# Kernel tuning notes

Hardware: AMD Instinct MI355X
Metric: run time of the kernel (lower is better)

Reference implementation:

```python
import jax, jax.numpy as jnp
import numpy as np
from jax import lax

B, T, H, W, C = 2, 32, 65, 65, 32
KS = 15   # kernel_size
F = 32    # conv features


def setup_inputs() -> dict:
    key = jax.random.key(0)
    ks = jax.random.split(key, 12)
    d = {}
    d["input_seq"] = jax.random.normal(ks[0], (B, T, H, W, C), jnp.float32)
    d["conv_w"] = jax.random.normal(ks[1], (3, 3, C, F), jnp.float32) / np.sqrt(3 * 3 * C).astype(np.float32)
    d["conv_b"] = jnp.zeros((F,), jnp.float32)
    for i, nm in enumerate(["alpha", "delta", "mu", "gamma"]):
        d[f"w_{nm}"] = jax.random.normal(ks[2 + i], (F, C), jnp.float32) / np.sqrt(F).astype(np.float32)
        d[f"b_{nm}"] = jnp.zeros((C,), jnp.float32)
    # nn.initializers.normal() -> stddev 0.01
    d["k_exc"] = jax.random.normal(ks[10], (KS, KS, C), jnp.float32) * 0.01
    d["k_inh"] = jax.random.normal(ks[11], (KS, KS, C), jnp.float32) * 0.01
    return d


def _kernel_spec(k, Hh, Ww):
    # zero-pad the (KS,KS,C) kernel to (H,W,C), then rfft2 over spatial axes
    ph, pw = (Hh - KS) // 2, (Ww - KS) // 2
    kp = jnp.pad(k, ((ph, ph), (pw, pw), (0, 0)))
    return jnp.fft.rfft2(kp, axes=(0, 1))  # (H, W//2+1, C) complex64


def reference(input_seq, conv_w, conv_b, w_alpha, b_alpha, w_delta, b_delta,
              w_mu, b_mu, w_gamma, b_gamma, k_exc, k_inh):
    Bb, Tt, Hh, Ww, Cc = input_seq.shape
    # context conv: flax Conv flattens leading (B,T) into batch; SAME, stride 2
    x = input_seq.reshape(Bb * Tt, Hh, Ww, Cc)
    stats = lax.conv_general_dilated(x, conv_w, (2, 2), 'SAME',
                                     dimension_numbers=('NHWC', 'HWIO', 'NHWC')) + conv_b
    stats = jax.nn.gelu(stats)  # flax nn.gelu (approximate)
    Hp, Wp = stats.shape[1], stats.shape[2]
    stats = stats.reshape(Bb, Tt, Hp, Wp, F)
    ctx = jnp.mean(stats, axis=(1, 2))                 # (B, Wp, F); Wp == W//2+1 for odd W
    alpha = jax.nn.sigmoid(ctx @ w_alpha + b_alpha)    # (B, Wp, C)
    delta = jax.nn.sigmoid(ctx @ w_delta + b_delta)
    mu = jax.nn.softplus(ctx @ w_mu + b_mu)
    gamma = jax.nn.softplus(ctx @ w_gamma + b_gamma)

    K_E = _kernel_spec(k_exc, Hh, Ww)  # (H, Wr, C)
    K_I = _kernel_spec(k_inh, Hh, Ww)
    Wr = Ww // 2 + 1
    decay = jnp.asarray(0.9, jnp.complex64)

    bc = lambda v: jnp.broadcast_to(v[:, None, :, :].astype(jnp.complex64), (Bb, Hh, Wr, Cc))
    A_xx = decay * bc(alpha)
    A_yy = decay * bc(delta)
    A_xy = -K_I[None] * bc(mu)
    A_yx = K_E[None] * bc(gamma)
    row0 = jnp.stack([A_xx, A_xy], axis=-1)
    row1 = jnp.stack([A_yx, A_yy], axis=-1)
    K_hat = jnp.stack([row0, row1], axis=-2)           # (B, H, Wr, C, 2, 2)

    U_hat = jnp.fft.rfft2(input_seq, axes=(2, 3))      # (B, T, H, Wr, C) complex64
    U_vec = jnp.stack([U_hat, jnp.zeros_like(U_hat)], axis=-1)  # (B,T,H,Wr,C,2)
    A_t = jnp.broadcast_to(K_hat[:, None], (Bb, Tt, Hh, Wr, Cc, 2, 2))

    # associative op for linear SSM: state_t = A_t @ state_{t-1} + u_t
    # (log/exp of the original cancel: exp(log A)=A, exp(State_log)=State)
    def combine(l, r):
        A1, b1 = l
        A2, b2 = r
        A = jnp.einsum('...ij,...jk->...ik', A2, A1)
        b = jnp.einsum('...ij,...j->...i', A2, b1) + b2
        return A, b

    _, S = lax.associative_scan(combine, (A_t, U_vec), axis=1)
    Y = S[..., 1]                                      # inhibitory component
    return jnp.fft.irfft2(Y, axes=(2, 3))              # (B, T, H, 2*(Wr-1), C) float32
```

## Files before the change

kernel.cpp:

```cpp
#include <hip/hip_runtime.h>
#include <cmath>

#define NB 2
#define NT 32
#define NH 65
#define NW 65
#define NC 32
#define NF 32
#define NKS 15
#define NHP 33
#define NWP 33
#define NWR 33
#define NWOUT 64
#define PI_F 3.14159265358979323846f

using bf16x8 = __attribute__((ext_vector_type(8))) __bf16;
using f32x4  = __attribute__((ext_vector_type(4))) float;
using s16x4  = __attribute__((ext_vector_type(4))) short;

__device__ inline unsigned short f2bf(float v) {
    unsigned u = __float_as_uint(v);
    u = u + 0x7FFF + ((u >> 16) & 1);
    return (unsigned short)(u >> 16);
}
__device__ inline float bf2f(unsigned short h) {
    return __uint_as_float((unsigned)h << 16);
}

union FragU { s16x4 h[2]; bf16x8 v; };

__global__ __launch_bounds__(256) void setup_kernel(
    const float* __restrict__ w, unsigned short* __restrict__ wBh,
    unsigned short* __restrict__ wBl,
    float2* __restrict__ twr, float2* __restrict__ twb, float2* __restrict__ twi,
    const float* __restrict__ kexc, const float* __restrict__ kinh,
    float2* __restrict__ KE, float2* __restrict__ KI)
{
    int blk = blockIdx.x;
    if (blk < 10) {
        int tid = blk * 256 + threadIdx.x;
        if (tid < NH * 36) {
            int q = tid / 36, wr = tid % 36;
            float2 v = make_float2(0.f, 0.f);
            if (wr < NWR) {
                int p = (q * wr) % NH;
                float a = -2.f * PI_F * (float)p / (float)NH;
                v = make_float2(cosf(a), sinf(a));
            }
            twr[tid] = v;
        }
        if (tid < NH * 14) {
            int h = tid / 14, b = tid % 14;
            float2 v = make_float2(0.f, 0.f);
            if (b < 13) {
                int p = (h * b) % NH;
                float a = 2.f * PI_F * (float)p / (float)NH;
                v = make_float2(cosf(a), sinf(a));
            }
            twb[tid] = v;
        }
        if (tid < 31 * 64) {
            int q = tid / 64 + 1, ow = tid % 64;
            int p = (q * ow) & 63;
            float a = 2.f * PI_F * (float)p / (float)NWOUT;
            twi[tid] = make_float2(cosf(a), sinf(a));
        }
    } else if (blk < 46) {
        int tid = (blk - 10) * 256 + threadIdx.x;
        if (tid < 9 * NF * NC) {
            int dd = tid / 1024;
            int f = (tid / 32) % 32;
            int c = tid % 32;
            float v = w[((size_t)dd * NC + c) * NF + f];
            unsigned short h = f2bf(v);
            wBh[tid] = h;
            wBl[tid] = f2bf(v - bf2f(h));
        }
    } else {
        __shared__ float2 tw[NH];
        int tid = threadIdx.x;
        if (tid < NH) {
            float a = -2.f * PI_F * (float)tid / (float)NH;
            tw[tid] = make_float2(cosf(a), sinf(a));
        }
        __syncthreads();
        int idx = (blk - 46) * 256 + tid;
        if (idx >= NH * NWR * NC) return;
        int c = idx % NC;
        int rem = idx / NC;
        int wr = rem % NWR;
        int h = rem / NWR;
        float ker = 0, kei = 0, kir = 0, kii = 0;
        int prow = (25 * (h + wr)) % NH;
        for (int i = 0; i < NKS; ++i) {
            int p = prow;
            for (int j = 0; j < NKS; ++j) {
                float2 e = tw[p];
                float ve = kexc[(i * NKS + j) * NC + c];
                float vi = kinh[(i * NKS + j) * NC + c];
                ker = fmaf(ve, e.x, ker); kei = fmaf(ve, e.y, kei);
                kir = fmaf(vi, e.x, kir); kii = fmaf(vi, e.y, kii);
                p += wr; if (p >= NH) p -= NH;
            }
            prow += h; if (prow >= NH) prow -= NH;
        }
        KE[idx] = make_float2(ker, kei);
        KI[idx] = make_float2(kir, kii);
    }
}

__global__ __launch_bounds__(256) void conv_mfma_kernel(
    const float* __restrict__ x, const unsigned short* __restrict__ wBh,
    const unsigned short* __restrict__ wBl, const float* __restrict__ bias,
    float* __restrict__ partial)
{
    __shared__ unsigned short aH[3 * 68 * 36];
    __shared__ unsigned short aL[3 * 68 * 36];
    int blk = blockIdx.x;
    int i = blk % NHP;
    int bt = blk / NHP;
    int tid = threadIdx.x;
    int l = tid & 63;
    int w = tid >> 6;

    int nt = w & 1;
    int fcol = nt * 16 + (l & 15);
    int c0 = (l >> 4) * 8;
    bf16x8 bh[9], bl[9];
    #pragma unroll
    for (int dd = 0; dd < 9; ++dd) {
        bh[dd] = *(const bf16x8*)(wBh + dd * 1024 + fcol * 32 + c0);
        bl[dd] = *(const bf16x8*)(wBl + dd * 1024 + fcol * 32 + c0);
    }

    const float* xb = x + (size_t)bt * (NH * NW * NC);
    for (int q = tid; q < 3 * 68 * 8; q += 256) {
        int r = q / 544;
        int k = q % 544;
        int pcol = k >> 3;
        int c4 = (k & 7) * 4;
        int gr = 2 * i - 1 + r;
        int gcol = pcol - 1;
        float4 v = make_float4(0.f, 0.f, 0.f, 0.f);
        if (gr >= 0 && gr < NH && gcol >= 0 && gcol < NW)
            v = *(const float4*)(xb + ((size_t)gr * NW + gcol) * NC + c4);
        int base = (r * 68 + pcol) * 36 + c4;
        unsigned short h0 = f2bf(v.x), h1 = f2bf(v.y), h2 = f2bf(v.z), h3 = f2bf(v.w);
        s16x4 th = {(short)h0, (short)h1, (short)h2, (short)h3};
        *(s16x4*)(aH + base) = th;
        s16x4 tl = {(short)f2bf(v.x - bf2f(h0)), (short)f2bf(v.y - bf2f(h1)),
                    (short)f2bf(v.z - bf2f(h2)), (short)f2bf(v.w - bf2f(h3))};
        *(s16x4*)(aL + base) = tl;
    }
    __syncthreads();

    float bv = bias[fcol];
    f32x4 acc0 = {bv, bv, bv, bv};
    f32x4 acc1 = {bv, bv, bv, bv};
    const int mtA = (w >> 1) ? 1 : 0;
    const bool hasB = (w >> 1) == 0;
    int m15 = l & 15;

    #pragma unroll
    for (int dd = 0; dd < 9; ++dd) {
        const int di = dd / 3, dj = dd % 3;
        {
            int pcol = 2 * (mtA * 16 + m15) + dj;
            int off = (di * 68 + pcol) * 36 + c0;
            FragU ah, al;
            ah.h[0] = *(const s16x4*)(aH + off);
            ah.h[1] = *(const s16x4*)(aH + off + 4);
            al.h[0] = *(const s16x4*)(aL + off);
            al.h[1] = *(const s16x4*)(aL + off + 4);
            acc0 = __builtin_amdgcn_mfma_f32_16x16x32_bf16(al.v, bh[dd], acc0, 0, 0, 0);
            acc0 = __builtin_amdgcn_mfma_f32_16x16x32_bf16(ah.v, bl[dd], acc0, 0, 0, 0);
            acc0 = __builtin_amdgcn_mfma_f32_16x16x32_bf16(ah.v, bh[dd], acc0, 0, 0, 0);
        }
        if (hasB) {
            int pcol = 2 * (32 + m15) + dj;
            if (pcol > 67) pcol = 67;
            int off = (di * 68 + pcol) * 36 + c0;
            FragU ah, al;
            ah.h[0] = *(const s16x4*)(aH + off);
            ah.h[1] = *(const s16x4*)(aH + off + 4);
            al.h[0] = *(const s16x4*)(aL + off);
            al.h[1] = *(const s16x4*)(aL + off + 4);
            acc1 = __builtin_amdgcn_mfma_f32_16x16x32_bf16(al.v, bh[dd], acc1, 0, 0, 0);
            acc1 = __builtin_amdgcn_mfma_f32_16x16x32_bf16(ah.v, bl[dd], acc1, 0, 0, 0);
            acc1 = __builtin_amdgcn_mfma_f32_16x16x32_bf16(ah.v, bh[dd], acc1, 0, 0, 0);
        }
    }

    float* pout = partial + (size_t)blk * (NWP * NF);
    int g4 = (l >> 4) * 4;
    #define GELU(v) (0.5f * (v) * (1.f + tanhf(0.7978845608028654f * ((v) + 0.044715f * (v) * (v) * (v)))))
    #pragma unroll
    for (int r = 0; r < 4; ++r) {
        float v = acc0[r];
        pout[(mtA * 16 + g4 + r) * NF + fcol] = GELU(v);
    }
    if (hasB && g4 == 0) {
        float v = acc1[0];
        pout[32 * NF + fcol] = GELU(v);
    }
    #undef GELU
}

__global__ __launch_bounds__(256) void ctx_reduce1_kernel(
    const float* __restrict__ partial, float* __restrict__ red2)
{
    __shared__ float red[4][64];
    int blk = blockIdx.x;
    int b = blk / 136;
    int rem = blk % 136;
    int chunk = rem / 8;
    int ts = rem % 8;
    int lane = threadIdx.x & 63;
    int tig = threadIdx.x >> 6;
    int jf = chunk * 64 + lane;
    float s0 = 0.f, s1 = 0.f, s2 = 0.f;
    if (jf < NWP * NF) {
        const float* p = partial + (size_t)b * (NT * NHP) * (NWP * NF)
                       + (size_t)(ts * 132 + tig * 33) * (NWP * NF) + jf;
        #pragma unroll 3
        for (int s = 0; s < 33; s += 3) {
            s0 += p[(size_t)s * (NWP * NF)];
            s1 += p[(size_t)(s + 1) * (NWP * NF)];
            s2 += p[(size_t)(s + 2) * (NWP * NF)];
        }
    }
    red[tig][lane] = s0 + s1 + s2;
    __syncthreads();
    if (threadIdx.x < 64) {
        float tot = red[0][threadIdx.x] + red[1][threadIdx.x] +
                    red[2][threadIdx.x] + red[3][threadIdx.x];
        red2[((b * 17 + chunk) * 8 + ts) * 64 + threadIdx.x] = tot;
    }
}

__global__ __launch_bounds__(256) void ctx_reduce2_kernel(
    const float* __restrict__ red2, float* __restrict__ ctx)
{
    __shared__ float red[4][64];
    int b = blockIdx.x / 17, chunk = blockIdx.x % 17;
    int lane = threadIdx.x & 63, tg = threadIdx.x >> 6;
    const float* r2 = red2 + ((size_t)(b * 17 + chunk) * 8) * 64;
    float v = r2[(2 * tg) * 64 + lane] + r2[(2 * tg + 1) * 64 + lane];
    red[tg][lane] = v;
    __syncthreads();
    if (threadIdx.x < 64) {
        int jf = chunk * 64 + threadIdx.x;
        if (jf < NWP * NF) {
            float tot = red[0][threadIdx.x] + red[1][threadIdx.x] +
                        red[2][threadIdx.x] + red[3][threadIdx.x];
            ctx[b * (NWP * NF) + jf] = tot * (1.f / (NT * NHP));
        }
    }
}

__global__ __launch_bounds__(256) void gate_kernel(
    const float* __restrict__ ctx,
    const float* __restrict__ wA, const float* __restrict__ bA,
    const float* __restrict__ wD, const float* __restrict__ bD,
    const float* __restrict__ wM, const float* __restrict__ bM,
    const float* __restrict__ wG, const float* __restrict__ bG,
    float* __restrict__ alpha, float* __restrict__ delta,
    float* __restrict__ mu, float* __restrict__ gamma)
{
    int idx = blockIdx.x * 256 + threadIdx.x;
    if (idx >= NB * NWP * NC) return;
    int c = idx % NC;
    int bw = idx / NC;
    float sA = bA[c], sD = bD[c], sM = bM[c], sG = bG[c];
    #pragma unroll
    for (int f = 0; f < NF; ++f) {
        float v = ctx[bw * NF + f];
        sA = fmaf(v, wA[f * NC + c], sA);
        sD = fmaf(v, wD[f * NC + c], sD);
        sM = fmaf(v, wM[f * NC + c], sM);
        sG = fmaf(v, wG[f * NC + c], sG);
    }
    alpha[idx] = 1.f / (1.f + expf(-sA));
    delta[idx] = 1.f / (1.f + expf(-sD));
    mu[idx]    = fmaxf(sM, 0.f) + log1pf(expf(-fabsf(sM)));
    gamma[idx] = fmaxf(sG, 0.f) + log1pf(expf(-fabsf(sG)));
}

__global__ __launch_bounds__(256) void dft_rows_kernel(
    const float* __restrict__ x, const float2* __restrict__ twr_g,
    float2* __restrict__ U1)
{
    __shared__ __align__(16) float row[4][NW * NC];
    __shared__ __align__(16) float2 twt[NH * 36];
    int tid = threadIdx.x;
    int blk = blockIdx.x;
    int grp = blk % 17;
    int bt = blk / 17;
    int hbase = grp * 4;
    int nrows = NH - hbase; if (nrows > 4) nrows = 4;

    const float* xp = x + ((size_t)bt * NH + hbase) * (NW * NC);
    for (int idx = tid; idx < nrows * NW * NC; idx += 256) ((float*)row)[idx] = xp[idx];
    for (int idx = tid; idx < NH * 36; idx += 256) twt[idx] = twr_g[idx];
    __syncthreads();

    int c = tid & 31;
    int jg = tid >> 5;
    float2 acc[4][4];
    #pragma unroll
    for (int r = 0; r < 4; ++r)
        #pragma unroll
        for (int k = 0; k < 4; ++k) acc[r][k] = make_float2(0.f, 0.f);

    const float2* tp = twt + 4 * jg;
    #pragma unroll 5
    for (int q = 0; q < NW; ++q) {
        float4 e01 = *(const float4*)&tp[q * 36];
        float4 e23 = *(const float4*)&tp[q * 36 + 2];
        #pragma unroll
        for (int r = 0; r < 4; ++r) {
            float v = row[r][q * NC + c];
            acc[r][0].x = fmaf(v, e01.x, acc[r][0].x); acc[r][0].y = fmaf(v, e01.y, acc[r][0].y);
            acc[r][1].x = fmaf(v, e01.z, acc[r][1].x); acc[r][1].y = fmaf(v, e01.w, acc[r][1].y);
            acc[r][2].x = fmaf(v, e23.x, acc[r][2].x); acc[r][2].y = fmaf(v, e23.y, acc[r][2].y);
            acc[r][3].x = fmaf(v, e23.z, acc[r][3].x); acc[r][3].y = fmaf(v, e23.w, acc[r][3].y);
        }
    }
    #pragma unroll
    for (int r = 0; r < 4; ++r) {
        if (r < nrows) {
            float2* up = U1 + ((size_t)bt * NH + hbase + r) * (NWR * NC);
            up[(4 * jg + 0) * NC + c] = acc[r][0];
            up[(4 * jg + 1) * NC + c] = acc[r][1];
            up[(4 * jg + 2) * NC + c] = acc[r][2];
            up[(4 * jg + 3) * NC + c] = acc[r][3];
        }
    }
    if (jg == 0) {
        float2 a32[4];
        #pragma unroll
        for (int r = 0; r < 4; ++r) a32[r] = make_float2(0.f, 0.f);
        #pragma unroll 5
        for (int q = 0; q < NW; ++q) {
            float2 e = twt[q * 36 + 32];
            #pragma unroll
            for (int r = 0; r < 4; ++r) {
                float v = row[r][q * NC + c];
                a32[r].x = fmaf(v, e.x, a32[r].x);
                a32[r].y = fmaf(v, e.y, a32[r].y);
            }
        }
        #pragma unroll
        for (int r = 0; r < 4; ++r)
            if (r < nrows)
                U1[((size_t)bt * NH + hbase + r) * (NWR * NC) + 32 * NC + c] = a32[r];
    }
}

template <int SIGN>
__device__ inline void compute5(const float2 v[5], float2* outp) {
    const float C5[5] = {1.f, 0.30901699437494742f, -0.80901699437494745f,
                         -0.80901699437494745f, 0.30901699437494742f};
    const float S5[5] = {0.f, 0.95105651629515357f, 0.58778525229247314f,
                         -0.58778525229247314f, -0.95105651629515357f};
    #pragma unroll
    for (int r = 0; r < 5; ++r) {
        float re = 0.f, im = 0.f;
        #pragma unroll
        for (int a = 0; a < 5; ++a) {
            const int m = (r * a) % 5;
            const float ex = C5[m];
            const float ey = (float)SIGN * S5[m];
            re = fmaf(v[a].x, ex, fmaf(-v[a].y, ey, re));
            im = fmaf(v[a].x, ey, fmaf(v[a].y, ex, im));
        }
        outp[r * NC] = make_float2(re, im);
    }
}

template <int SIGN, bool SCALE>
__global__ __launch_bounds__(256) void dft_cols_kernel(
    const float2* __restrict__ in, float2* __restrict__ out,
    const float2* __restrict__ twb_g)
{
    __shared__ __align__(16) float2 col[NH * NC];
    __shared__ __align__(16) float2 twb[NH * 14];
    int tid = threadIdx.x;
    int blk = blockIdx.x;
    int wr = blk % NWR;
    int bt = blk / NWR;
    const float2* ip = in + ((size_t)bt * NH) * (NWR * NC) + wr * NC;
    for (int idx = tid; idx < NH * NC; idx += 256) {
        int p = idx >> 5, c = idx & 31;
        col[idx] = ip[(size_t)p * (NWR * NC) + c];
    }
    for (int idx = tid; idx < NH * 14; idx += 256) twb[idx] = twb_g[idx];
    __syncthreads();

    float2 va0[5], va1[5];
    int bq0 = tid >> 5, c0 = tid & 31;
    int q1 = tid + 256;
    int bq1 = q1 >> 5, c1 = q1 & 31;
    #pragma unroll
    for (int a = 0; a < 5; ++a) {
        va0[a] = col[(13 * a + bq0) * NC + c0];
        if (q1 < 416) va1[a] = col[(13 * a + bq1) * NC + c1];
    }
    __syncthreads();
    compute5<SIGN>(va0, &col[(bq0 * 5) * NC + c0]);
    if (q1 < 416) compute5<SIGN>(va1, &col[(bq1 * 5) * NC + c1]);
    __syncthreads();

    const float S = (float)SIGN;
    int c = tid & 31;
    int h0 = tid >> 5;
    const float s = SCALE ? (1.f / (float)NH) : 1.f;
    float2* op = out + ((size_t)bt * NH) * (NWR * NC) + wr * NC;
    float2 acc[8];
    #pragma unroll
    for (int k = 0; k < 8; ++k) {
        int h = h0 + 8 * k;
        int r = h % 5;
        const float2* Ap = col + r * NC + c;
        const float2* tp = twb + h * 14;
        float re = 0.f, im = 0.f;
        #pragma unroll
        for (int p = 0; p < 6; ++p) {
            float4 tq = *(const float4*)&tp[2 * p];
            float2 v0 = Ap[(2 * p) * 5 * NC];
            float2 v1 = Ap[(2 * p + 1) * 5 * NC];
            re = fmaf(v0.x, tq.x, fmaf(-S * v0.y, tq.y, re));
            im = fmaf(S * v0.x, tq.y, fmaf(v0.y, tq.x, im));
            re = fmaf(v1.x, tq.z, fmaf(-S * v1.y, tq.w, re));
            im = fmaf(S * v1.x, tq.w, fmaf(v1.y, tq.z, im));
        }
        {
            float2 t12 = tp[12];
            float2 v = Ap[12 * 5 * NC];
            re = fmaf(v.x, t12.x, fmaf(-S * v.y, t12.y, re));
            im = fmaf(S * v.x, t12.y, fmaf(v.y, t12.x, im));
        }
        acc[k] = make_float2(re * s, im * s);
    }
    #pragma unroll
    for (int k = 0; k < 8; ++k) {
        int h = h0 + 8 * k;
        op[(size_t)h * (NWR * NC) + c] = acc[k];
    }
    if (h0 == 0) {
        const float2* Ap = col + 4 * NC + c;
        const float2* tp = twb + 64 * 14;
        float re = 0.f, im = 0.f;
        #pragma unroll
        for (int p = 0; p < 6; ++p) {
            float4 tq = *(const float4*)&tp[2 * p];
            float2 v0 = Ap[(2 * p) * 5 * NC];
            float2 v1 = Ap[(2 * p + 1) * 5 * NC];
            re = fmaf(v0.x, tq.x, fmaf(-S * v0.y, tq.y, re));
            im = fmaf(S * v0.x, tq.y, fmaf(v0.y, tq.x, im));
            re = fmaf(v1.x, tq.z, fmaf(-S * v1.y, tq.w, re));
            im = fmaf(S * v1.x, tq.w, fmaf(v1.y, tq.z, im));
        }
        {
            float2 t12 = tp[12];
            float2 v = Ap[12 * 5 * NC];
            re = fmaf(v.x, t12.x, fmaf(-S * v.y, t12.y, re));
            im = fmaf(S * v.x, t12.y, fmaf(v.y, t12.x, im));
        }
        op[(size_t)64 * (NWR * NC) + c] = make_float2(re * s, im * s);
    }
}

__global__ __launch_bounds__(256) void scan_kernel(
    float2* __restrict__ buf, const float2* __restrict__ KE,
    const float2* __restrict__ KI, const float* __restrict__ alpha,
    const float* __restrict__ delta, const float* __restrict__ mu,
    const float* __restrict__ gamma)
{
    int idx = blockIdx.x * 256 + threadIdx.x;
    if (idx >= NB * NH * NWR * NC) return;
    int c = idx % NC;
    int rem = idx / NC;
    int wr = rem % NWR;
    int rem2 = rem / NWR;
    int h = rem2 % NH;
    int b = rem2 / NH;

    int gi = (b * NWP + wr) * NC + c;
    float axx = 0.9f * alpha[gi];
    float ayy = 0.9f * delta[gi];
    float m = mu[gi], g = gamma[gi];
    float2 ki = KI[(h * NWR + wr) * NC + c];
    float2 ke = KE[(h * NWR + wr) * NC + c];
    float2 axy = make_float2(-ki.x * m, -ki.y * m);
    float2 ayx = make_float2(ke.x * g, ke.y * g);

    float2 xs = make_float2(0.f, 0.f), ys = make_float2(0.f, 0.f);
    size_t base = ((size_t)b * NT) * NH * NWR * NC + (size_t)h * (NWR * NC) + wr * NC + c;
    const size_t stride = (size_t)NH * NWR * NC;
    for (int t = 0; t < NT; ++t) {
        float2 U = buf[base + (size_t)t * stride];
        float2 nx, ny;
        nx.x = fmaf(axx, xs.x, fmaf(axy.x, ys.x, fmaf(-axy.y, ys.y, U.x)));
        nx.y = fmaf(axx, xs.y, fmaf(axy.x, ys.y, fmaf(axy.y, ys.x, U.y)));
        ny.x = fmaf(ayx.x, xs.x, fmaf(-ayx.y, xs.y, ayy * ys.x));
        ny.y = fmaf(ayx.x, xs.y, fmaf(ayx.y, xs.x, ayy * ys.y));
        xs = nx; ys = ny;
        buf[base + (size_t)t * stride] = ys;
    }
}

__global__ __launch_bounds__(256) void irfft_w_kernel(
    const float2* __restrict__ Z, const float2* __restrict__ twi_g,
    float* __restrict__ out)
{
    __shared__ __align__(16) float2 z[4][NWR * NC];
    __shared__ __align__(16) float2 twi[31 * 64];
    int tid = threadIdx.x;
    int blk = blockIdx.x;
    int grp = blk % 17;
    int bt = blk / 17;
    int hbase = grp * 4;
    int nrows = NH - hbase; if (nrows > 4) nrows = 4;

    const float2* zp = Z + ((size_t)bt * NH + hbase) * (NWR * NC);
    for (int idx = tid; idx < nrows * NWR * NC; idx += 256) ((float2*)z)[idx] = zp[idx];
    for (int idx = tid; idx < 31 * 64; idx += 256) twi[idx] = twi_g[idx];
    __syncthreads();

    int c = tid & 31;
    int g = tid >> 5;
    float acc[4][8];
    #pragma unroll
    for (int r = 0; r < 4; ++r) {
        float z0 = z[r][c].x;
        float zn = z[r][32 * NC + c].x;
        #pragma unroll
        for (int m = 0; m < 8; ++m) acc[r][m] = z0 + ((m & 1) ? -zn : zn);
    }
    const float2* tp = twi + 8 * g;
    for (int q = 1; q < 32; ++q) {
        const float4* tq = (const float4*)&tp[(q - 1) * 64];
        float4 e0 = tq[0], e1 = tq[1], e2 = tq[2], e3 = tq[3];
        #pragma unroll
        for (int r = 0; r < 4; ++r) {
            float2 v = z[r][q * NC + c];
            float vx = 2.f * v.x, vy = 2.f * v.y;
            acc[r][0] = fmaf(vx, e0.x, fmaf(-vy, e0.y, acc[r][0]));
            acc[r][1] = fmaf(vx, e0.z, fmaf(-vy, e0.w, acc[r][1]));
            acc[r][2] = fmaf(vx, e1.x, fmaf(-vy, e1.y, acc[r][2]));
            acc[r][3] = fmaf(vx, e1.z, fmaf(-vy, e1.w, acc[r][3]));
            acc[r][4] = fmaf(vx, e2.x, fmaf(-vy, e2.y, acc[r][4]));
            acc[r][5] = fmaf(vx, e2.z, fmaf(-vy, e2.w, acc[r][5]));
            acc[r][6] = fmaf(vx, e3.x, fmaf(-vy, e3.y, acc[r][6]));
            acc[r][7] = fmaf(vx, e3.z, fmaf(-vy, e3.w, acc[r][7]));
        }
    }
    #pragma unroll
    for (int r = 0; r < 4; ++r) {
        if (r < nrows) {
            float* op = out + ((size_t)bt * NH + hbase + r) * (NWOUT * NC);
            #pragma unroll
            for (int m = 0; m < 8; ++m)
                op[(8 * g + m) * NC + c] = acc[r][m] * (1.f / (float)NWOUT);
        }
    }
}

extern "C" void kernel_launch(void* const* d_in, const int* in_sizes, int n_in,
                              void* d_out, int out_size, void* d_ws, size_t ws_size,
                              hipStream_t stream)
{
    const float* x     = (const float*)d_in[0];
    const float* convw = (const float*)d_in[1];
    const float* convb = (const float*)d_in[2];
    const float* wA = (const float*)d_in[3];
    const float* bA = (const float*)d_in[4];
    const float* wD = (const float*)d_in[5];
    const float* bD = (const float*)d_in[6];
    const float* wM = (const float*)d_in[7];
    const float* bM = (const float*)d_in[8];
    const float* wG = (const float*)d_in[9];
    const float* bG = (const float*)d_in[10];
    const float* kexc = (const float*)d_in[11];
    const float* kinh = (const float*)d_in[12];

    const size_t NBIG = (size_t)NB * NT * NH * NWR * NC;
    char* ws = (char*)d_ws;
    float2* bufA    = (float2*)ws;  ws += NBIG * sizeof(float2);
    float2* KE      = (float2*)ws;  ws += (size_t)NH * NWR * NC * sizeof(float2);
    float2* KI      = (float2*)ws;  ws += (size_t)NH * NWR * NC * sizeof(float2);
    float*  partial = (float*)ws;   ws += (size_t)NB * (NT * NHP) * (NWP * NF) * sizeof(float);
    float*  ctx     = (float*)ws;   ws += (size_t)NB * NWP * NF * sizeof(float);
    float*  red2    = (float*)ws;   ws += (size_t)NB * 17 * 8 * 64 * sizeof(float);
    float*  alpha   = (float*)ws;   ws += (size_t)NB * NWP * NC * sizeof(float);
    float*  delta   = (float*)ws;   ws += (size_t)NB * NWP * NC * sizeof(float);
    float*  mu      = (float*)ws;   ws += (size_t)NB * NWP * NC * sizeof(float);
    float*  gamma   = (float*)ws;   ws += (size_t)NB * NWP * NC * sizeof(float);
    float2* TWR     = (float2*)ws;  ws += (size_t)NH * 36 * sizeof(float2);
    float2* TWB     = (float2*)ws;  ws += (size_t)NH * 14 * sizeof(float2);
    float2* TWI     = (float2*)ws;  ws += (size_t)31 * 64 * sizeof(float2);
    unsigned short* wBh = (unsigned short*)ws; ws += (size_t)9 * NC * NF * sizeof(unsigned short);
    unsigned short* wBl = (unsigned short*)ws; ws += (size_t)9 * NC * NF * sizeof(unsigned short);

    const int specBlocks = (NH * NWR * NC + 255) / 256;
    setup_kernel<<<46 + specBlocks, 256, 0, stream>>>(
        convw, wBh, wBl, TWR, TWB, TWI, kexc, kinh, KE, KI);

    conv_mfma_kernel<<<NB * NT * NHP, 256, 0, stream>>>(x, wBh, wBl, convb, partial);
    ctx_reduce1_kernel<<<NB * 136, 256, 0, stream>>>(partial, red2);
    ctx_reduce2_kernel<<<NB * 17, 256, 0, stream>>>(red2, ctx);
    gate_kernel<<<(NB * NWP * NC + 255) / 256, 256, 0, stream>>>(
        ctx, wA, bA, wD, bD, wM, bM, wG, bG, alpha, delta, mu, gamma);

    dft_rows_kernel<<<NB * NT * 17, 256, 0, stream>>>(x, TWR, bufA);
    dft_cols_kernel<-1, false><<<NB * NT * NWR, 256, 0, stream>>>(bufA, bufA, TWB);

    scan_kernel<<<(NB * NH * NWR * NC + 255) / 256, 256, 0, stream>>>(
        bufA, KE, KI, alpha, delta, mu, gamma);

    dft_cols_kernel<+1, true><<<NB * NT * NWR, 256, 0, stream>>>(bufA, bufA, TWB);
    irfft_w_kernel<<<NB * NT * 17, 256, 0, stream>>>(bufA, TWI, (float*)d_out);
}
```

Before: 168.8 us.

## Replace column DFT with split-bf16 MFMA matrix multiply over 65-point axis

The hand-written 5x13 factored column DFT on CUDA cores is replaced by a dense DFT matmul on MFMA units. Setup precomputes hi/lo bf16 split tables of the cos and ±sin DFT matrix, padded to 80x96. Each block converts its column data into hi/lo bf16 in shared memory, and four waves compute 16x16 output tiles with three-product split-bf16 accumulation to keep near-fp32 accuracy. This trades more raw FLOPs (a dense DFT instead of a factored one, plus 12 MFMAs per k-tile) for tensor-core throughput. It also adds bf16 conversion overhead and some precision risk.

```diff
diff --git a/kernel.cpp b/kernel.cpp
--- a/kernel.cpp
+++ b/kernel.cpp
@@ -32,9 +32,10 @@
 __global__ __launch_bounds__(256) void setup_kernel(
     const float* __restrict__ w, unsigned short* __restrict__ wBh,
     unsigned short* __restrict__ wBl,
-    float2* __restrict__ twr, float2* __restrict__ twb, float2* __restrict__ twi,
+    float2* __restrict__ twr, float2* __restrict__ twi,
     const float* __restrict__ kexc, const float* __restrict__ kinh,
-    float2* __restrict__ KE, float2* __restrict__ KI)
+    float2* __restrict__ KE, float2* __restrict__ KI,
+    unsigned short* __restrict__ Atab)
 {
     int blk = blockIdx.x;
     if (blk < 10) {
@@ -49,16 +50,6 @@
             }
             twr[tid] = v;
         }
-        if (tid < NH * 14) {
-            int h = tid / 14, b = tid % 14;
-            float2 v = make_float2(0.f, 0.f);
-            if (b < 13) {
-                int p = (h * b) % NH;
-                float a = 2.f * PI_F * (float)p / (float)NH;
-                v = make_float2(cosf(a), sinf(a));
-            }
-            twb[tid] = v;
-        }
         if (tid < 31 * 64) {
             int q = tid / 64 + 1, ow = tid % 64;
             int p = (q * ow) & 63;
@@ -76,7 +67,7 @@
             wBh[tid] = h;
             wBl[tid] = f2bf(v - bf2f(h));
         }
-    } else {
+    } else if (blk < 315) {
         __shared__ float2 tw[NH];
         int tid = threadIdx.x;
         if (tid < NH) {
@@ -106,6 +97,27 @@
         }
         KE[idx] = make_float2(ker, kei);
         KI[idx] = make_float2(kir, kii);
+    } else {
+        int idx = (blk - 315) * 256 + threadIdx.x;
+        if (idx >= 46080) return;
+        int tbl = idx / 7680;
+        int rem = idx % 7680;
+        int mt = rem / 1536;
+        int rem2 = rem % 1536;
+        int kt = rem2 / 512;
+        int rem3 = rem2 % 512;
+        int lane = rem3 / 8;
+        int e = rem3 % 8;
+        int m = mt * 16 + (lane & 15);
+        int k = kt * 32 + (lane >> 4) * 8 + e;
+        unsigned short out = 0;
+        if (m < NH && k < NH) {
+            float a = 2.f * PI_F * (float)((m * k) % NH) / (float)NH;
+            float base = (tbl < 2) ? cosf(a) : ((tbl < 4) ? sinf(a) : -sinf(a));
+            unsigned short hi = f2bf(base);
+            out = (tbl & 1) ? f2bf(base - bf2f(hi)) : hi;
+        }
+        Atab[idx] = out;
     }
 }
 
@@ -357,117 +369,80 @@
     }
 }
 
-template <int SIGN>
-__device__ inline void compute5(const float2 v[5], float2* outp) {
-    const float C5[5] = {1.f, 0.30901699437494742f, -0.80901699437494745f,
-                         -0.80901699437494745f, 0.30901699437494742f};
-    const float S5[5] = {0.f, 0.95105651629515357f, 0.58778525229247314f,
-                         -0.58778525229247314f, -0.95105651629515357f};
-    #pragma unroll
-    for (int r = 0; r < 5; ++r) {
-        float re = 0.f, im = 0.f;
-        #pragma unroll
-        for (int a = 0; a < 5; ++a) {
-            const int m = (r * a) % 5;
-            const float ex = C5[m];
-            const float ey = (float)SIGN * S5[m];
-            re = fmaf(v[a].x, ex, fmaf(-v[a].y, ey, re));
-            im = fmaf(v[a].x, ey, fmaf(v[a].y, ex, im));
-        }
-        outp[r * NC] = make_float2(re, im);
-    }
-}
-
-template <int SIGN, bool SCALE>
-__global__ __launch_bounds__(256) void dft_cols_kernel(
+template <int DIR>
+__global__ __launch_bounds__(256) void dft_cols_mfma_kernel(
     const float2* __restrict__ in, float2* __restrict__ out,
-    const float2* __restrict__ twb_g)
-{
-    __shared__ __align__(16) float2 col[NH * NC];
-    __shared__ __align__(16) float2 twb[NH * 14];
+    const unsigned short* __restrict__ Atab)
+{
+    __shared__ __align__(16) unsigned short Xt[4][32][104];
     int tid = threadIdx.x;
     int blk = blockIdx.x;
     int wr = blk % NWR;
     int bt = blk / NWR;
     const float2* ip = in + ((size_t)bt * NH) * (NWR * NC) + wr * NC;
-    for (int idx = tid; idx < NH * NC; idx += 256) {
+
+    for (int idx = tid; idx < 96 * 32; idx += 256) {
         int p = idx >> 5, c = idx & 31;
-        col[idx] = ip[(size_t)p * (NWR * NC) + c];
-    }
-    for (int idx = tid; idx < NH * 14; idx += 256) twb[idx] = twb_g[idx];
+        float2 v = make_float2(0.f, 0.f);
+        if (p < NH) v = ip[(size_t)p * (NWR * NC) + c];
+        unsigned short rh = f2bf(v.x);
+        unsigned short ih = f2bf(v.y);
+        Xt[0][c][p] = rh;
+        Xt[1][c][p] = f2bf(v.x - bf2f(rh));
+        Xt[2][c][p] = ih;
+        Xt[3][c][p] = f2bf(v.y - bf2f(ih));
+    }
     __syncthreads();
 
-    float2 va0[5], va1[5];
-    int bq0 = tid >> 5, c0 = tid & 31;
-    int q1 = tid + 256;
-    int bq1 = q1 >> 5, c1 = q1 & 31;
-    #pragma unroll
-    for (int a = 0; a < 5; ++a) {
-        va0[a] = col[(13 * a + bq0) * NC + c0];
-        if (q1 < 416) va1[a] = col[(13 * a + bq1) * NC + c1];
-    }
-    __syncthreads();
-    compute5<SIGN>(va0, &col[(bq0 * 5) * NC + c0]);
-    if (q1 < 416) compute5<SIGN>(va1, &col[(bq1 * 5) * NC + c1]);
-    __syncthreads();
-
-    const float S = (float)SIGN;
-    int c = tid & 31;
-    int h0 = tid >> 5;
-    const float s = SCALE ? (1.f / (float)NH) : 1.f;
+    int l = tid & 63;
+    int w = tid >> 6;
+    int lm = l & 15;
+    int lk = (l >> 4) * 8;
+    const float scale = DIR ? (1.f / (float)NH) : 1.f;
     float2* op = out + ((size_t)bt * NH) * (NWR * NC) + wr * NC;
-    float2 acc[8];
-    #pragma unroll
-    for (int k = 0; k < 8; ++k) {
-        int h = h0 + 8 * k;
-        int r = h % 5;
-        const float2* Ap = col + r * NC + c;
-        const float2* tp = twb + h * 14;
-        float re = 0.f, im = 0.f;
-        #pragma unroll
-        for (int p = 0; p < 6; ++p) {
-            float4 tq = *(const float4*)&tp[2 * p];
-            float2 v0 = Ap[(2 * p) * 5 * NC];
-            float2 v1 = Ap[(2 * p + 1) * 5 * NC];
-            re = fmaf(v0.x, tq.x, fmaf(-S * v0.y, tq.y, re));
-            im = fmaf(S * v0.x, tq.y, fmaf(v0.y, tq.x, im));
-            re = fmaf(v1.x, tq.z, fmaf(-S * v1.y, tq.w, re));
-            im = fmaf(S * v1.x, tq.w, fmaf(v1.y, tq.z, im));
-        }
-        {
-            float2 t12 = tp[12];
-            float2 v = Ap[12 * 5 * NC];
-            re = fmaf(v.x, t12.x, fmaf(-S * v.y, t12.y, re));
-            im = fmaf(S * v.x, t12.y, fmaf(v.y, t12.x, im));
-        }
-        acc[k] = make_float2(re * s, im * s);
-    }
-    #pragma unroll
-    for (int k = 0; k < 8; ++k) {
-        int h = h0 + 8 * k;
-        op[(size_t)h * (NWR * NC) + c] = acc[k];
-    }
-    if (h0 == 0) {
-        const float2* Ap = col + 4 * NC + c;
-        const float2* tp = twb + 64 * 14;
-        float re = 0.f, im = 0.f;
-        #pragma unroll
-        for (int p = 0; p < 6; ++p) {
-            float4 tq = *(const float4*)&tp[2 * p];
-            float2 v0 = Ap[(2 * p) * 5 * NC];
-            float2 v1 = Ap[(2 * p + 1) * 5 * NC];
-            re = fmaf(v0.x, tq.x, fmaf(-S * v0.y, tq.y, re));
-            im = fmaf(S * v0.x, tq.y, fmaf(v0.y, tq.x, im));
-            re = fmaf(v1.x, tq.z, fmaf(-S * v1.y, tq.w, re));
-            im = fmaf(S * v1.x, tq.w, fmaf(v1.y, tq.z, im));
-        }
-        {
-            float2 t12 = tp[12];
-            float2 v = Ap[12 * 5 * NC];
-            re = fmaf(v.x, t12.x, fmaf(-S * v.y, t12.y, re));
-            im = fmaf(S * v.x, t12.y, fmaf(v.y, t12.x, im));
-        }
-        op[(size_t)64 * (NWR * NC) + c] = make_float2(re * s, im * s);
+
+    for (int pr = w; pr < 10; pr += 4) {
+        int mt = pr >> 1, nt = pr & 1;
+        f32x4 accr = {0.f, 0.f, 0.f, 0.f};
+        f32x4 acci = {0.f, 0.f, 0.f, 0.f};
+        #pragma unroll
+        for (int kt = 0; kt < 3; ++kt) {
+            const unsigned short* ab = Atab + ((size_t)mt * 3 + kt) * 512 + l * 8;
+            bf16x8 Ch  = *(const bf16x8*)(ab + 0 * 7680);
+            bf16x8 Cl  = *(const bf16x8*)(ab + 1 * 7680);
+            bf16x8 Sph = *(const bf16x8*)(ab + 2 * 7680);
+            bf16x8 Spl = *(const bf16x8*)(ab + 3 * 7680);
+            bf16x8 Snh = *(const bf16x8*)(ab + 4 * 7680);
+            bf16x8 Snl = *(const bf16x8*)(ab + 5 * 7680);
+            bf16x8 S1h = DIR ? Snh : Sph, S1l = DIR ? Snl : Spl;
+            bf16x8 S2h = DIR ? Sph : Snh, S2l = DIR ? Spl : Snl;
+            int n = nt * 16 + lm;
+            int k = kt * 32 + lk;
+            bf16x8 Xrh = *(const bf16x8*)&Xt[0][n][k];
+            bf16x8 Xrl = *(const bf16x8*)&Xt[1][n][k];
+            bf16x8 Xih = *(const bf16x8*)&Xt[2][n][k];
+            bf16x8 Xil = *(const bf16x8*)&Xt[3][n][k];
+            accr = __builtin_amdgcn_mfma_f32_16x16x32_bf16(Cl,  Xrh, accr, 0, 0, 0);
+            accr = __builtin_amdgcn_mfma_f32_16x16x32_bf16(Ch,  Xrl, accr, 0, 0, 0);
+            accr = __builtin_amdgcn_mfma_f32_16x16x32_bf16(Ch,  Xrh, accr, 0, 0, 0);
+            accr = __builtin_amdgcn_mfma_f32_16x16x32_bf16(S1l, Xih, accr, 0, 0, 0);
+            accr = __builtin_amdgcn_mfma_f32_16x16x32_bf16(S1h, Xil, accr, 0, 0, 0);
+            accr = __builtin_amdgcn_mfma_f32_16x16x32_bf16(S1h, Xih, accr, 0, 0, 0);
+            acci = __builtin_amdgcn_mfma_f32_16x16x32_bf16(Cl,  Xih, acci, 0, 0, 0);
+            acci = __builtin_amdgcn_mfma_f32_16x16x32_bf16(Ch,  Xil, acci, 0, 0, 0);
+            acci = __builtin_amdgcn_mfma_f32_16x16x32_bf16(Ch,  Xih, acci, 0, 0, 0);
+            acci = __builtin_amdgcn_mfma_f32_16x16x32_bf16(S2l, Xrh, acci, 0, 0, 0);
+            acci = __builtin_amdgcn_mfma_f32_16x16x32_bf16(S2h, Xrl, acci, 0, 0, 0);
+            acci = __builtin_amdgcn_mfma_f32_16x16x32_bf16(S2h, Xrh, acci, 0, 0, 0);
+        }
+        int c = nt * 16 + lm;
+        #pragma unroll
+        for (int r = 0; r < 4; ++r) {
+            int m = mt * 16 + (l >> 4) * 4 + r;
+            if (m < NH)
+                op[(size_t)m * (NWR * NC) + c] =
+                    make_float2(accr[r] * scale, acci[r] * scale);
+        }
     }
 }
 
@@ -598,14 +573,13 @@
     float*  mu      = (float*)ws;   ws += (size_t)NB * NWP * NC * sizeof(float);
     float*  gamma   = (float*)ws;   ws += (size_t)NB * NWP * NC * sizeof(float);
     float2* TWR     = (float2*)ws;  ws += (size_t)NH * 36 * sizeof(float2);
-    float2* TWB     = (float2*)ws;  ws += (size_t)NH * 14 * sizeof(float2);
     float2* TWI     = (float2*)ws;  ws += (size_t)31 * 64 * sizeof(float2);
     unsigned short* wBh = (unsigned short*)ws; ws += (size_t)9 * NC * NF * sizeof(unsigned short);
     unsigned short* wBl = (unsigned short*)ws; ws += (size_t)9 * NC * NF * sizeof(unsigned short);
-
-    const int specBlocks = (NH * NWR * NC + 255) / 256;
-    setup_kernel<<<46 + specBlocks, 256, 0, stream>>>(
-        convw, wBh, wBl, TWR, TWB, TWI, kexc, kinh, KE, KI);
+    unsigned short* Atab = (unsigned short*)ws; ws += (size_t)46080 * sizeof(unsigned short);
+
+    setup_kernel<<<495, 256, 0, stream>>>(
+        convw, wBh, wBl, TWR, TWI, kexc, kinh, KE, KI, Atab);
 
     conv_mfma_kernel<<<NB * NT * NHP, 256, 0, stream>>>(x, wBh, wBl, convb, partial);
     ctx_reduce1_kernel<<<NB * 136, 256, 0, stream>>>(partial, red2);
@@ -614,11 +588,11 @@
         ctx, wA, bA, wD, bD, wM, bM, wG, bG, alpha, delta, mu, gamma);
 
     dft_rows_kernel<<<NB * NT * 17, 256, 0, stream>>>(x, TWR, bufA);
-    dft_cols_kernel<-1, false><<<NB * NT * NWR, 256, 0, stream>>>(bufA, bufA, TWB);
+    dft_cols_mfma_kernel<0><<<NB * NT * NWR, 256, 0, stream>>>(bufA, bufA, Atab);
 
     scan_kernel<<<(NB * NH * NWR * NC + 255) / 256, 256, 0, stream>>>(
         bufA, KE, KI, alpha, delta, mu, gamma);
 
-    dft_cols_kernel<+1, true><<<NB * NT * NWR, 256, 0, stream>>>(bufA, bufA, TWB);
+    dft_cols_mfma_kernel<1><<<NB * NT * NWR, 256, 0, stream>>>(bufA, bufA, Atab);
     irfft_w_kernel<<<NB * NT * 17, 256, 0, stream>>>(bufA, TWI, (float*)d_out);
 }
```

After: 183.2 us. 1.09x slower.
